# Kernel tuning notes

Measured on AMD Instinct MI355X. Metric: run time of the kernel, lower is better.

The kernel has to match this reference:

```python
import jax, jax.numpy as jnp
import numpy as np
import math

D_MODEL = 512
N_HEADS = 8
D_FF = 2048
TOP_FACTOR = 5
LN_EPS = 1e-5


def _layernorm(x, g, b):
    m = jnp.mean(x, axis=-1, keepdims=True)
    v = jnp.mean((x - m) ** 2, axis=-1, keepdims=True)
    return (x - m) / jnp.sqrt(v + LN_EPS) * g + b


def _prob_sparse_attn(q_in, k_in, v_in, wq, bq, wk, bk, wv, bv, wo, bo):
    # weights stored (in, out): y = x @ w + b  (equivalent to torch Linear)
    B, Lq, dm = q_in.shape
    Lk = k_in.shape[1]
    H, D = N_HEADS, dm // N_HEADS
    q = (q_in @ wq + bq).reshape(B, Lq, H, D).transpose(0, 2, 1, 3)  # (B,H,Lq,D)
    k = (k_in @ wk + bk).reshape(B, Lk, H, D).transpose(0, 2, 1, 3)
    v = (v_in @ wv + bv).reshape(B, Lk, H, D).transpose(0, 2, 1, 3)

    qn = q / jnp.linalg.norm(q, axis=-1, keepdims=True)
    kn = k / jnp.linalg.norm(k, axis=-1, keepdims=True)
    # full cosine-similarity matrix, reduced to a row mean (as in the original)
    scores_all = jnp.einsum('bhqd,bhkd->bhqk', qn, kn)
    mean_scores = scores_all.mean(axis=-1)  # (B,H,Lq)

    u = max(1, Lq // TOP_FACTOR)
    _, top_idx = jax.lax.top_k(mean_scores, u)  # (B,H,u)

    q_sel = jnp.take_along_axis(q, top_idx[..., None], axis=2)  # (B,H,u,D)
    scores = jnp.einsum('bhud,bhkd->bhuk', q_sel, k) / math.sqrt(D)
    attn = jax.nn.softmax(scores, axis=-1)
    ctx_sel = jnp.einsum('bhuk,bhkd->bhud', attn, v)  # (B,H,u,D)

    b_ix = jnp.arange(B)[:, None, None]
    h_ix = jnp.arange(H)[None, :, None]
    context = jnp.zeros((B, H, Lq, D), dtype=q.dtype).at[b_ix, h_ix, top_idx].set(ctx_sel)
    out = context.transpose(0, 2, 1, 3).reshape(B, Lq, dm)
    return out @ wo + bo


def _decoder_layer(x, enc_out, p):
    xn = _layernorm(x, p['ln1_g'], p['ln1_b'])
    x = x + _prob_sparse_attn(xn, xn, xn, p['sa_wq'], p['sa_bq'], p['sa_wk'], p['sa_bk'],
                              p['sa_wv'], p['sa_bv'], p['sa_wo'], p['sa_bo'])
    xn = _layernorm(x, p['ln2_g'], p['ln2_b'])
    x = x + _prob_sparse_attn(xn, enc_out, enc_out, p['ca_wq'], p['ca_bq'], p['ca_wk'], p['ca_bk'],
                              p['ca_wv'], p['ca_bv'], p['ca_wo'], p['ca_bo'])
    xn = _layernorm(x, p['ln3_g'], p['ln3_b'])
    h = jax.nn.relu(xn @ p['ff_w1'] + p['ff_b1'])
    return x + (h @ p['ff_w2'] + p['ff_b2'])


def setup_inputs() -> dict:
    key = jax.random.key(0)
    ks = iter(jax.random.split(key, 32))
    B, L = 2, 2048
    dm, dff = D_MODEL, D_FF
    s = 1.0 / math.sqrt(dm)
    inp = {
        'x': jax.random.normal(next(ks), (B, L, dm), jnp.float32),
        'enc_out': jax.random.normal(next(ks), (B, L, dm), jnp.float32),
    }
    for pre in ('sa', 'ca'):
        for nm in ('wq', 'wk', 'wv', 'wo'):
            inp[f'{pre}_{nm}'] = jax.random.normal(next(ks), (dm, dm), jnp.float32) * s
            inp[f'{pre}_{nm[1:] and "b" + nm[1:]}'] = jnp.zeros((dm,), jnp.float32)
    inp['ff_w1'] = jax.random.normal(next(ks), (dm, dff), jnp.float32) * s
    inp['ff_b1'] = jnp.zeros((dff,), jnp.float32)
    inp['ff_w2'] = jax.random.normal(next(ks), (dff, dm), jnp.float32) / math.sqrt(dff)
    inp['ff_b2'] = jnp.zeros((dm,), jnp.float32)
    for i in (1, 2, 3):
        inp[f'ln{i}_g'] = jnp.ones((dm,), jnp.float32)
        inp[f'ln{i}_b'] = jnp.zeros((dm,), jnp.float32)
    return inp


def reference(x, enc_out,
              sa_wq, sa_bq, sa_wk, sa_bk, sa_wv, sa_bv, sa_wo, sa_bo,
              ca_wq, ca_bq, ca_wk, ca_bk, ca_wv, ca_bv, ca_wo, ca_bo,
              ff_w1, ff_b1, ff_w2, ff_b2,
              ln1_g, ln1_b, ln2_g, ln2_b, ln3_g, ln3_b):
    p = dict(sa_wq=sa_wq, sa_bq=sa_bq, sa_wk=sa_wk, sa_bk=sa_bk, sa_wv=sa_wv, sa_bv=sa_bv,
             sa_wo=sa_wo, sa_bo=sa_bo, ca_wq=ca_wq, ca_bq=ca_bq, ca_wk=ca_wk, ca_bk=ca_bk,
             ca_wv=ca_wv, ca_bv=ca_bv, ca_wo=ca_wo, ca_bo=ca_bo,
             ff_w1=ff_w1, ff_b1=ff_b1, ff_w2=ff_w2, ff_b2=ff_b2,
             ln1_g=ln1_g, ln1_b=ln1_b, ln2_g=ln2_g, ln2_b=ln2_b, ln3_g=ln3_g, ln3_b=ln3_b)
    return _decoder_layer(x, enc_out, p)
```

## Files before the change

### kernel.cpp

```cpp
#include <hip/hip_runtime.h>

#define BB 2
#define LL 2048
#define DM 512
#define NH 8
#define DH 64
#define DFF 2048
#define UU 409
#define ROWS (BB*LL)
#define X_ELEMS 2097152
#define IN_TOTAL 8398336
#define NCHUNK 16

typedef unsigned short u16;
typedef __attribute__((ext_vector_type(8))) short short8;
typedef __attribute__((ext_vector_type(4))) float floatx4;

#define G_TOTAL 34700000
__device__ float g_buf[G_TOTAL];
__device__ int   g_isbf16;

#define A_XN    8398336
#define A_Q     10495488
#define A_K     12592640
#define A_V     14689792
#define A_CTX   16786944
#define A_ENC   18884096
#define A_H     20981248
#define A_MKN   23078400
#define A_MS    23079424
#define A_SEL   23112192
#define A_PARTK 23144960
#define A_LIST  23177728
#define A_PART2 23184384
#define A_WT    30426112
#define XN_H    16796672
#define XN_L    18893824
#define CTX_H   33573888
#define CTX_L   35671040
#define ENC_H   37768192
#define ENC_L   39865344
#define AH_H    41962496
#define WT_SAQKV 60852224
#define WT_SAO   62425088
#define WT_CAQ   62949376
#define WT_CAKV  63473664
#define WT_CAO   64522240
#define WT_W1    65046528
#define WT_W2    67143680

__constant__ int c_end[28] = {
    2097152, 4194304, 4456448, 4456960, 4719104, 4719616, 4981760, 4982272,
    5244416, 5244928, 5507072, 5507584, 5769728, 5770240, 6032384, 6032896,
    6295040, 6295552, 7344128, 7346176, 8394752, 8395264, 8395776, 8396288,
    8396800, 8397312, 8397824, 8398336
};

__device__ __forceinline__ float bf2f(u16 x) {
    union { unsigned int u; float f; } c; c.u = ((unsigned int)x) << 16; return c.f;
}
__device__ __forceinline__ u16 f2bf(float f) {
    union { float f; unsigned int u; } c; c.f = f;
    unsigned int u = c.u;
    return (u16)((u + 0x7FFFu + ((u >> 16) & 1u)) >> 16);
}

struct P28 { const void* p[28]; };
struct I3 { int v[3]; };
__global__ void cvt_all(P28 ps) {
    const int f = (((const u16*)ps.p[22])[0] == 0x3F80u) ? 1 : 0;
    if (blockIdx.x == 0 && threadIdx.x == 0) g_isbf16 = f;
    int stride = gridDim.x * blockDim.x;
    u16* gb16 = (u16*)g_buf;
    for (int idx = blockIdx.x * blockDim.x + threadIdx.x; idx < IN_TOTAL; idx += stride) {
        int s = 0;
        while (idx >= c_end[s]) s++;
        int start = (s == 0) ? 0 : c_end[s - 1];
        int local = idx - start;
        float v;
        if (f) v = bf2f(((const u16*)ps.p[s])[local]);
        else   v = ((const float*)ps.p[s])[local];
        g_buf[idx] = v;
        if (s == 1) {
            u16 hi = f2bf(v);
            gb16[ENC_H + local] = hi;
            gb16[ENC_L + local] = f2bf(v - bf2f(hi));
        }
    }
}

__constant__ int tj[10][6] = {
    {4194304, WT_SAQKV, 0,    512,  786432, 8},
    {4456960, WT_SAQKV, 512,  512,  786432, 8},
    {4719616, WT_SAQKV, 1024, 512,  786432, 8},
    {4982272, WT_SAO,   0,    512,  262144, 8},
    {5244928, WT_CAQ,   0,    512,  262144, 8},
    {5507584, WT_CAKV,  0,    512,  524288, 8},
    {5770240, WT_CAKV,  512,  512,  524288, 8},
    {6032896, WT_CAO,   0,    512,  262144, 8},
    {6295552, WT_W1,    0,    512, 1048576, 32},
    {7346176, WT_W2,    0,   2048, 1048576, 8},
};
__constant__ int tcum[10] = {64, 128, 192, 256, 320, 384, 448, 512, 768, 1024};
__global__ void transpose_all() {
    int bid = blockIdx.x;
    int j = 0;
    while (bid >= tcum[j]) j++;
    int t = bid - (j ? tcum[j - 1] : 0);
    int w_off = tj[j][0], wt = tj[j][1], col0 = tj[j][2];
    int K = tj[j][3], lo = tj[j][4], txn = tj[j][5];
    int Nsrc = txn * 64;
    int n0 = (t % txn) * 64, k0 = (t / txn) * 64;
    __shared__ float tb[64][65];
    int c = threadIdx.x & 63, r0 = threadIdx.x >> 6;
    const float* W = g_buf + w_off;
    u16* WTh = ((u16*)g_buf) + wt;
    for (int i = 0; i < 16; i++) {
        int r = r0 + 4 * i;
        tb[r][c] = W[(size_t)(k0 + r) * Nsrc + n0 + c];
    }
    __syncthreads();
    for (int i = 0; i < 16; i++) {
        int r = r0 + 4 * i;
        float v = tb[c][r];
        u16 hi = f2bf(v);
        size_t o = (size_t)(col0 + n0 + r) * K + k0 + c;
        WTh[o] = hi;
        WTh[lo + o] = f2bf(v - bf2f(hi));
    }
}

__global__ void lnorm_k(int x_off, int g_off, int b_off, int yh_u16, int yl_u16) {
    int row = blockIdx.x;
    int tid = threadIdx.x;
    const float* x = g_buf + x_off + (size_t)row * DM;
    float a = x[tid], c = x[tid + 256];
    float s1 = a + c, s2 = a * a + c * c;
    for (int o = 32; o > 0; o >>= 1) { s1 += __shfl_xor(s1, o); s2 += __shfl_xor(s2, o); }
    __shared__ float r1[4], r2[4];
    int wave = tid >> 6, lane = tid & 63;
    if (lane == 0) { r1[wave] = s1; r2[wave] = s2; }
    __syncthreads();
    s1 = r1[0] + r1[1] + r1[2] + r1[3];
    s2 = r2[0] + r2[1] + r2[2] + r2[3];
    float mean = s1 * (1.0f / DM);
    float var  = s2 * (1.0f / DM) - mean * mean;
    float rstd = rsqrtf(var + 1e-5f);
    const float* gg = g_buf + g_off;
    const float* bb = g_buf + b_off;
    u16* yh = ((u16*)g_buf) + yh_u16 + (size_t)row * DM;
    u16* yl = ((u16*)g_buf) + yl_u16 + (size_t)row * DM;
    float v1 = (a - mean) * rstd * gg[tid]       + bb[tid];
    float v2 = (c - mean) * rstd * gg[tid + 256] + bb[tid + 256];
    u16 h1 = f2bf(v1), h2 = f2bf(v2);
    yh[tid] = h1;       yl[tid] = f2bf(v1 - bf2f(h1));
    yh[tid + 256] = h2; yl[tid + 256] = f2bf(v2 - bf2f(h2));
}

template<int WM, bool SPLIT, bool SEC, bool RELU, bool RESID, bool FINAL, bool OUTH>
__global__ void mgemm_k(int a_u16, int wt_u16_off, I3 boffs, int resid_off,
                        int out_off, void* __restrict__ dext, int M, int N, int K) {
    constexpr int BT_M = WM * 32;
    __shared__ u16 Ash[BT_M * 40];
    __shared__ u16 Asl[SPLIT ? BT_M * 40 : 8];
    __shared__ u16 Bsh[128 * 40];
    __shared__ u16 Bsl[SPLIT ? 128 * 40 : 8];
    const u16* Ah = ((const u16*)g_buf) + a_u16;
    const u16* Al = Ah + (size_t)M * K;
    const u16* WTh = ((const u16*)g_buf) + wt_u16_off;
    const u16* WTl = WTh + (size_t)N * K;
    int isbf = FINAL ? g_isbf16 : 0;
    int tid = threadIdx.x;
    int lane = tid & 63, wid = tid >> 6;
    int wm = wid >> 1, wn = wid & 1;
    int quad = lane >> 4, l15 = lane & 15;
    int m0 = blockIdx.y * BT_M, n0 = blockIdx.x * 128;
    floatx4 acc[WM][4];
#pragma unroll
    for (int i = 0; i < WM; i++)
#pragma unroll
        for (int j = 0; j < 4; j++) acc[i][j] = (floatx4){0.f, 0.f, 0.f, 0.f};
    for (int k0 = 0; k0 < K; k0 += 32) {
#pragma unroll
        for (int i = 0; i < WM / 2; i++) {
            int idx8 = tid + 256 * i;
            int r = idx8 >> 2, c8 = (idx8 & 3) * 8;
            *(uint4*)(&Ash[r * 40 + c8]) = *(const uint4*)(Ah + (size_t)(m0 + r) * K + k0 + c8);
            if constexpr (SPLIT)
                *(uint4*)(&Asl[r * 40 + c8]) = *(const uint4*)(Al + (size_t)(m0 + r) * K + k0 + c8);
        }
#pragma unroll
        for (int i = 0; i < 2; i++) {
            int idx8 = tid + 256 * i;
            int r = idx8 >> 2, c8 = (idx8 & 3) * 8;
            *(uint4*)(&Bsh[r * 40 + c8]) = *(const uint4*)(WTh + (size_t)(n0 + r) * K + k0 + c8);
            if constexpr (SPLIT)
                *(uint4*)(&Bsl[r * 40 + c8]) = *(const uint4*)(WTl + (size_t)(n0 + r) * K + k0 + c8);
        }
        __syncthreads();
        short8 ah[WM], bh[4], al[WM], bl[4];
#pragma unroll
        for (int i = 0; i < WM; i++) {
            int ro = (wm * WM * 16 + i * 16 + l15) * 40 + quad * 8;
            ah[i] = *(const short8*)(&Ash[ro]);
            if constexpr (SPLIT) al[i] = *(const short8*)(&Asl[ro]);
        }
#pragma unroll
        for (int j = 0; j < 4; j++) {
            int ro = (wn * 64 + j * 16 + l15) * 40 + quad * 8;
            bh[j] = *(const short8*)(&Bsh[ro]);
            if constexpr (SPLIT) bl[j] = *(const short8*)(&Bsl[ro]);
        }
#pragma unroll
        for (int i = 0; i < WM; i++)
#pragma unroll
            for (int j = 0; j < 4; j++) {
                acc[i][j] = __builtin_amdgcn_mfma_f32_16x16x32_bf16(ah[i], bh[j], acc[i][j], 0, 0, 0);
                if constexpr (SPLIT) {
                    acc[i][j] = __builtin_amdgcn_mfma_f32_16x16x32_bf16(ah[i], bl[j], acc[i][j], 0, 0, 0);
                    acc[i][j] = __builtin_amdgcn_mfma_f32_16x16x32_bf16(al[i], bh[j], acc[i][j], 0, 0, 0);
                }
            }
        __syncthreads();
    }
#pragma unroll
    for (int i = 0; i < WM; i++)
#pragma unroll
        for (int j = 0; j < 4; j++)
#pragma unroll
            for (int r = 0; r < 4; r++) {
                int row = m0 + wm * WM * 16 + i * 16 + quad * 4 + r;
                int col = n0 + wn * 64 + j * 16 + l15;
                int sec = SEC ? (col >> 9) : 0;
                int ci  = SEC ? (col & 511) : col;
                float v = acc[i][j][r] + g_buf[boffs.v[sec] + ci];
                if (RELU) v = fmaxf(v, 0.f);
                if (RESID) v += g_buf[resid_off + (size_t)row * N + col];
                if (FINAL) {
                    if (isbf) ((u16*)dext)[(size_t)row * N + col] = f2bf(v);
                    else      ((float*)dext)[(size_t)row * N + col] = v;
                } else if (OUTH) {
                    ((u16*)g_buf)[out_off + (size_t)row * N + col] = f2bf(v);
                } else if (SEC) {
                    g_buf[out_off + ((size_t)sec * M + row) * 512 + ci] = v;
                } else {
                    g_buf[out_off + (size_t)row * N + col] = v;
                }
            }
}

__global__ void meankn_p1(int k_off, int part_off) {
    int bh = blockIdx.x >> 5, chunk = blockIdx.x & 31;
    int b = bh >> 3, h = bh & 7;
    int wave = threadIdx.x >> 6, lane = threadIdx.x & 63;
    const float* base = g_buf + k_off + (size_t)b * LL * DM + (size_t)h * DH + lane;
    float acc = 0.f;
    for (int t = 0; t < 16; t++) {
        int j = chunk * 64 + wave * 16 + t;
        float kv = base[(size_t)j * DM];
        float s = kv * kv;
        for (int o = 32; o > 0; o >>= 1) s += __shfl_xor(s, o);
        acc += kv / sqrtf(fmaxf(s, 1e-30f));
    }
    __shared__ float red[4][64];
    red[wave][lane] = acc;
    __syncthreads();
    if (threadIdx.x < 64)
        g_buf[part_off + (size_t)blockIdx.x * 64 + threadIdx.x] =
            red[0][threadIdx.x] + red[1][threadIdx.x] + red[2][threadIdx.x] + red[3][threadIdx.x];
}
__global__ void meankn_p2(int part_off, int mkn_off) {
    int bh = blockIdx.x; int lane = threadIdx.x;
    float s = 0.f;
    for (int c = 0; c < 32; c++) s += g_buf[part_off + (size_t)(bh * 32 + c) * 64 + lane];
    g_buf[mkn_off + bh * 64 + lane] = s * (1.0f / LL);
}

__global__ void mscore_k(int q_off, int mkn_off, int ms_off) {
    int row = blockIdx.x * 4 + (threadIdx.x >> 6);
    int lane = threadIdx.x & 63;
    int q = row & (LL - 1);
    int bh = row >> 11;
    int b = bh >> 3, h = bh & 7;
    float qv = g_buf[q_off + ((size_t)b * LL + q) * DM + h * DH + lane];
    float m = g_buf[mkn_off + bh * 64 + lane];
    float s = qv * qv, d = qv * m;
    for (int o = 32; o > 0; o >>= 1) { s += __shfl_xor(s, o); d += __shfl_xor(d, o); }
    if (lane == 0) g_buf[ms_off + row] = d / sqrtf(fmaxf(s, 1e-30f));
}

__global__ void topsel_k(int ms_off, int sel_off, int u) {
    __shared__ float s[LL];
    int bh = blockIdx.y, chunk = blockIdx.x;
    for (int i = threadIdx.x; i < LL; i += 256) s[i] = g_buf[ms_off + bh * LL + i];
    __syncthreads();
    int il = threadIdx.x >> 2;
    int i = chunk * 64 + il;
    int jq = threadIdx.x & 3;
    float si = s[i];
    int cnt = 0;
    for (int t = 0; t < 512; t++) {
        int j = jq * 512 + t;
        float sj = s[j];
        cnt += (sj > si) || (sj == si && j < i);
    }
    cnt += __shfl_xor(cnt, 1);
    cnt += __shfl_xor(cnt, 2);
    if (jq == 0) ((int*)(g_buf + sel_off))[bh * LL + i] = (cnt < u) ? 1 : 0;
}

__global__ void compact_k(int sel_off, int list_off) {
    __shared__ int cnts[256];
    __shared__ int pref[256];
    int bh = blockIdx.x, tid = threadIdx.x;
    const int* sel = (const int*)(g_buf + sel_off) + bh * LL;
    int* list = (int*)(g_buf + list_off) + bh * 416;
    int c = 0;
    for (int j = 0; j < 8; j++) c += sel[tid * 8 + j];
    cnts[tid] = c;
    __syncthreads();
    if (tid == 0) { int run = 0; for (int i = 0; i < 256; i++) { pref[i] = run; run += cnts[i]; } }
    __syncthreads();
    int base = pref[tid];
    for (int j = 0; j < 8; j++) {
        int i = tid * 8 + j;
        if (sel[i]) list[base++] = i;
    }
}

__global__ void zero_k(int off, int n) {
    int i = blockIdx.x * blockDim.x + threadIdx.x;
    int st = gridDim.x * blockDim.x;
    for (; i < n; i += st) g_buf[off + i] = 0.f;
}

__global__ void attn_flash(int q_off, int k_off, int v_off, int list_off, int part_off, int u) {
    int bh = blockIdx.y, b = bh >> 3, h = bh & 7;
    int chunk = blockIdx.z;
    int tid = threadIdx.x, lane = tid & 63, w = tid >> 6;
    int quad = lane >> 4, l15 = lane & 15;
    const int* list = (const int*)(g_buf + list_off);

    int slot_q = blockIdx.x * 64 + w * 16 + l15;
    int qidx = list[bh * 416 + (slot_q < u ? slot_q : u - 1)];
    const float* qp = g_buf + q_off + ((size_t)b * LL + qidx) * DM + h * DH;
    short8 qh[2], ql[2];
#pragma unroll
    for (int d2 = 0; d2 < 2; d2++) {
        float v[8] __attribute__((aligned(16)));
        *(float4*)(v)     = *(const float4*)(qp + d2 * 32 + quad * 8);
        *(float4*)(v + 4) = *(const float4*)(qp + d2 * 32 + quad * 8 + 4);
        u16 hh[8] __attribute__((aligned(16)));
        u16 lo[8] __attribute__((aligned(16)));
#pragma unroll
        for (int j = 0; j < 8; j++) {
            float s = v[j] * 0.125f;
            u16 hi = f2bf(s); hh[j] = hi; lo[j] = f2bf(s - bf2f(hi));
        }
        qh[d2] = *(const short8*)hh; ql[d2] = *(const short8*)lo;
    }

    __shared__ u16 Ksh[64 * 72], Ksl[64 * 72];
    __shared__ u16 Vth[64 * 72], Vtl[64 * 72];
    __shared__ float Ps[4][16 * 68];

    float m_run[4] = {-3.0e38f, -3.0e38f, -3.0e38f, -3.0e38f};
    float l_run[4] = {0.f, 0.f, 0.f, 0.f};
    floatx4 acc_o[4];
#pragma unroll
    for (int j = 0; j < 4; j++) acc_o[j] = (floatx4){0.f, 0.f, 0.f, 0.f};

    for (int kt = 0; kt < 2; kt++) {
        int row0 = chunk * 128 + kt * 64;
        {
            int r = tid >> 2, c = (tid & 3) * 16;
            const float* kp = g_buf + k_off + ((size_t)b * LL + row0 + r) * DM + h * DH + c;
            float v[16] __attribute__((aligned(16)));
            *(float4*)(v)      = *(const float4*)(kp);
            *(float4*)(v + 4)  = *(const float4*)(kp + 4);
            *(float4*)(v + 8)  = *(const float4*)(kp + 8);
            *(float4*)(v + 12) = *(const float4*)(kp + 12);
            u16 hh[16] __attribute__((aligned(16)));
            u16 lo[16] __attribute__((aligned(16)));
#pragma unroll
            for (int j = 0; j < 16; j++) { u16 hi = f2bf(v[j]); hh[j] = hi; lo[j] = f2bf(v[j] - bf2f(hi)); }
            *(uint4*)(&Ksh[r * 72 + c])     = ((const uint4*)hh)[0];
            *(uint4*)(&Ksh[r * 72 + c + 8]) = ((const uint4*)hh)[1];
            *(uint4*)(&Ksl[r * 72 + c])     = ((const uint4*)lo)[0];
            *(uint4*)(&Ksl[r * 72 + c + 8]) = ((const uint4*)lo)[1];
        }
#pragma unroll
        for (int it = 0; it < 2; it++) {
            int sl = it * 256 + tid;
            int d = sl & 63, oct = sl >> 6;
            const float* vp = g_buf + v_off + ((size_t)b * LL + row0 + oct * 8) * DM + h * DH + d;
            u16 hh[8] __attribute__((aligned(16)));
            u16 lo[8] __attribute__((aligned(16)));
#pragma unroll
            for (int i = 0; i < 8; i++) {
                float x = vp[(size_t)i * DM];
                u16 hi = f2bf(x); hh[i] = hi; lo[i] = f2bf(x - bf2f(hi));
            }
            *(uint4*)(&Vth[d * 72 + oct * 8]) = *(const uint4*)hh;
            *(uint4*)(&Vtl[d * 72 + oct * 8]) = *(const uint4*)lo;
        }
        __syncthreads();
        floatx4 sacc[4];
#pragma unroll
        for (int t = 0; t < 4; t++) {
            sacc[t] = (floatx4){0.f, 0.f, 0.f, 0.f};
#pragma unroll
            for (int d2 = 0; d2 < 2; d2++) {
                int ro = (t * 16 + l15) * 72 + d2 * 32 + quad * 8;
                short8 kh = *(const short8*)(&Ksh[ro]);
                short8 kl = *(const short8*)(&Ksl[ro]);
                sacc[t] = __builtin_amdgcn_mfma_f32_16x16x32_bf16(qh[d2], kh, sacc[t], 0, 0, 0);
                sacc[t] = __builtin_amdgcn_mfma_f32_16x16x32_bf16(qh[d2], kl, sacc[t], 0, 0, 0);
                sacc[t] = __builtin_amdgcn_mfma_f32_16x16x32_bf16(ql[d2], kh, sacc[t], 0, 0, 0);
            }
        }
        float alpha[4];
#pragma unroll
        for (int r = 0; r < 4; r++) {
            float mx = fmaxf(fmaxf(sacc[0][r], sacc[1][r]), fmaxf(sacc[2][r], sacc[3][r]));
            for (int o = 1; o < 16; o <<= 1) mx = fmaxf(mx, __shfl_xor(mx, o));
            float mn = fmaxf(m_run[r], mx);
            alpha[r] = __expf(m_run[r] - mn);
            m_run[r] = mn;
            float ls = 0.f;
#pragma unroll
            for (int t = 0; t < 4; t++) {
                float p = __expf(sacc[t][r] - mn);
                sacc[t][r] = p;
                ls += p;
            }
            for (int o = 1; o < 16; o <<= 1) ls += __shfl_xor(ls, o);
            l_run[r] = l_run[r] * alpha[r] + ls;
        }
#pragma unroll
        for (int t = 0; t < 4; t++)
#pragma unroll
            for (int r = 0; r < 4; r++)
                Ps[w][(quad * 4 + r) * 68 + t * 16 + l15] = sacc[t][r];
#pragma unroll
        for (int j = 0; j < 4; j++)
#pragma unroll
            for (int r = 0; r < 4; r++) acc_o[j][r] *= alpha[r];
#pragma unroll
        for (int s2 = 0; s2 < 2; s2++) {
            float pv[8] __attribute__((aligned(16)));
            *(float4*)(pv)     = *(const float4*)(&Ps[w][l15 * 68 + s2 * 32 + quad * 8]);
            *(float4*)(pv + 4) = *(const float4*)(&Ps[w][l15 * 68 + s2 * 32 + quad * 8 + 4]);
            u16 ph[8] __attribute__((aligned(16)));
            u16 pl[8] __attribute__((aligned(16)));
#pragma unroll
            for (int j = 0; j < 8; j++) { u16 hi = f2bf(pv[j]); ph[j] = hi; pl[j] = f2bf(pv[j] - bf2f(hi)); }
            short8 phv = *(const short8*)ph, plv = *(const short8*)pl;
#pragma unroll
            for (int j = 0; j < 4; j++) {
                int ro = (j * 16 + l15) * 72 + s2 * 32 + quad * 8;
                short8 vh = *(const short8*)(&Vth[ro]);
                short8 vl = *(const short8*)(&Vtl[ro]);
                acc_o[j] = __builtin_amdgcn_mfma_f32_16x16x32_bf16(phv, vh, acc_o[j], 0, 0, 0);
                acc_o[j] = __builtin_amdgcn_mfma_f32_16x16x32_bf16(phv, vl, acc_o[j], 0, 0, 0);
                acc_o[j] = __builtin_amdgcn_mfma_f32_16x16x32_bf16(plv, vh, acc_o[j], 0, 0, 0);
            }
        }
        __syncthreads();
    }
#pragma unroll
    for (int r = 0; r < 4; r++) {
        int slot = blockIdx.x * 64 + w * 16 + quad * 4 + r;
        if (slot >= u) continue;
        float* pp = g_buf + part_off + (((size_t)bh * 416 + slot) * NCHUNK + chunk) * 68;
#pragma unroll
        for (int j = 0; j < 4; j++) pp[j * 16 + l15] = acc_o[j][r];
        if (l15 == 0) { pp[64] = m_run[r]; pp[65] = l_run[r]; }
    }
}

__global__ void attn_combine(int part_off, int list_off, int u) {
    int bh = blockIdx.y;
    int b = bh >> 3, h = bh & 7;
    int tid = threadIdx.x;
    int qi = tid >> 4;
    int kb = tid & 15;
    int ds = kb * 4;
    int slot = blockIdx.x * 16 + qi;
    if (slot >= u) return;
    int qidx = ((const int*)(g_buf + list_off))[bh * 416 + slot];
    const float* pp = g_buf + part_off + ((size_t)bh * 416 + slot) * NCHUNK * 68;
    float m = -3.0e38f;
#pragma unroll
    for (int c = 0; c < NCHUNK; c++) m = fmaxf(m, pp[c * 68 + 64]);
    float l = 0.f, O0 = 0.f, O1 = 0.f, O2 = 0.f, O3 = 0.f;
#pragma unroll
    for (int c = 0; c < NCHUNK; c++) {
        float a = __expf(pp[c * 68 + 64] - m);
        l += a * pp[c * 68 + 65];
        float4 o = *(const float4*)(pp + c * 68 + ds);
        O0 += a * o.x; O1 += a * o.y; O2 += a * o.z; O3 += a * o.w;
    }
    float inv = 1.0f / l;
    float o0 = O0 * inv, o1 = O1 * inv, o2 = O2 * inv, o3 = O3 * inv;
    size_t idx = ((size_t)b * LL + qidx) * DM + h * DH + ds;
    ushort4 hv, lv;
    hv.x = f2bf(o0); lv.x = f2bf(o0 - bf2f(hv.x));
    hv.y = f2bf(o1); lv.y = f2bf(o1 - bf2f(hv.y));
    hv.z = f2bf(o2); lv.z = f2bf(o2 - bf2f(hv.z));
    hv.w = f2bf(o3); lv.w = f2bf(o3 - bf2f(hv.w));
    *(ushort4*)(((u16*)g_buf) + CTX_H + idx) = hv;
    *(ushort4*)(((u16*)g_buf) + CTX_L + idx) = lv;
}

extern "C" void kernel_launch(void* const* d_in, const int* in_sizes, int n_in,
                              void* d_out, int out_size, void* d_ws, size_t ws_size,
                              hipStream_t stream) {
    static const int SZ[28] = {
        2097152, 2097152,
        262144, 512, 262144, 512, 262144, 512, 262144, 512,
        262144, 512, 262144, 512, 262144, 512, 262144, 512,
        1048576, 2048, 1048576, 512,
        512, 512, 512, 512, 512, 512
    };
    int OFF[28];
    int cur = 0;
    for (int i = 0; i < 28; i++) { OFF[i] = cur; cur += SZ[i]; }
    const int X = X_ELEMS;

    P28 ps;
    for (int i = 0; i < 28; i++) ps.p[i] = d_in[i];
    cvt_all<<<4096, 256, 0, stream>>>(ps);
    transpose_all<<<1024, 256, 0, stream>>>();

    auto select_attend = [&](void) {
        meankn_p1<<<16 * 32, 256, 0, stream>>>(A_K, A_PARTK);
        meankn_p2<<<16, 64, 0, stream>>>(A_PARTK, A_MKN);
        mscore_k<<<(BB * NH * LL) / 4, 256, 0, stream>>>(A_Q, A_MKN, A_MS);
        topsel_k<<<dim3(32, 16), 256, 0, stream>>>(A_MS, A_SEL, UU);
        compact_k<<<BB * NH, 256, 0, stream>>>(A_SEL, A_LIST);
        zero_k<<<1024, 256, 0, stream>>>(A_CTX, X);
        attn_flash<<<dim3(7, 16, NCHUNK), 256, 0, stream>>>(A_Q, A_K, A_V, A_LIST, A_PART2, UU);
        attn_combine<<<dim3(26, 16), 256, 0, stream>>>(A_PART2, A_LIST, UU);
    };

    lnorm_k<<<ROWS, 256, 0, stream>>>(OFF[0], OFF[22], OFF[23], XN_H, XN_L);
    mgemm_k<2, true, true, false, false, false, false><<<dim3(12, 64), 256, 0, stream>>>(
        XN_H, WT_SAQKV, I3{{OFF[3], OFF[5], OFF[7]}}, 0, A_Q, nullptr, ROWS, 1536, 512);
    select_attend();
    mgemm_k<2, true, false, false, true, false, false><<<dim3(4, 64), 256, 0, stream>>>(
        CTX_H, WT_SAO, I3{{OFF[9], 0, 0}}, OFF[0], OFF[0], nullptr, ROWS, 512, 512);

    lnorm_k<<<ROWS, 256, 0, stream>>>(OFF[0], OFF[24], OFF[25], XN_H, XN_L);
    mgemm_k<2, true, false, false, false, false, false><<<dim3(4, 64), 256, 0, stream>>>(
        XN_H, WT_CAQ, I3{{OFF[11], 0, 0}}, 0, A_Q, nullptr, ROWS, 512, 512);
    mgemm_k<2, true, true, false, false, false, false><<<dim3(8, 64), 256, 0, stream>>>(
        ENC_H, WT_CAKV, I3{{OFF[13], OFF[15], 0}}, 0, A_K, nullptr, ROWS, 1024, 512);
    select_attend();
    mgemm_k<2, false, false, false, true, false, false><<<dim3(4, 64), 256, 0, stream>>>(
        CTX_H, WT_CAO, I3{{OFF[17], 0, 0}}, OFF[0], OFF[0], nullptr, ROWS, 512, 512);

    lnorm_k<<<ROWS, 256, 0, stream>>>(OFF[0], OFF[26], OFF[27], XN_H, XN_L);
    mgemm_k<4, false, false, true, false, false, true><<<dim3(16, 32), 256, 0, stream>>>(
        XN_H, WT_W1, I3{{OFF[19], 0, 0}}, 0, AH_H, nullptr, ROWS, 2048, 512);
    mgemm_k<2, false, false, false, true, true, false><<<dim3(4, 64), 256, 0, stream>>>(
        AH_H, WT_W2, I3{{OFF[21], 0, 0}}, OFF[0], 0, d_out, ROWS, 512, 2048);
}
```

Measured before the change: 591.4 us.

## Precompute split-bf16 K and transposed V once; widen attention blocks; shrink GEMM M-tiles

Adds a prep kernel that converts K into hi/lo bf16 pairs and V into transposed hi/lo bf16 once per head. Before this, each attention chunk block repeated that conversion and did strided V loads for every query group. The flash kernel now handles two 16-query groups per wave (128 queries per block), so each K/V tile staged in shared memory is reused across twice as many queries, and it loads the precomputed tiles with vector copies. The N=512 GEMMs switch to 32-row tiles to get more blocks onto the device. The cost is extra global buffers, one more launch per attention, higher register pressure in the flash kernel, and fewer attention blocks.

```diff
diff --git a/kernel.cpp b/kernel.cpp
--- a/kernel.cpp
+++ b/kernel.cpp
@@ -16,7 +16,7 @@
 typedef __attribute__((ext_vector_type(8))) short short8;
 typedef __attribute__((ext_vector_type(4))) float floatx4;
 
-#define G_TOTAL 34700000
+#define G_TOTAL 38900000
 __device__ float g_buf[G_TOTAL];
 __device__ int   g_isbf16;
 
@@ -48,6 +48,10 @@
 #define WT_CAO   64522240
 #define WT_W1    65046528
 #define WT_W2    67143680
+#define KH_U    69240832
+#define KL_U    71337984
+#define VTH_U   73435136
+#define VTL_U   75532288
 
 __constant__ int c_end[28] = {
     2097152, 4194304, 4456448, 4456960, 4719104, 4719616, 4981760, 4982272,
@@ -161,6 +165,7 @@
 __global__ void mgemm_k(int a_u16, int wt_u16_off, I3 boffs, int resid_off,
                         int out_off, void* __restrict__ dext, int M, int N, int K) {
     constexpr int BT_M = WM * 32;
+    constexpr int A4 = BT_M * 4;
     __shared__ u16 Ash[BT_M * 40];
     __shared__ u16 Asl[SPLIT ? BT_M * 40 : 8];
     __shared__ u16 Bsh[128 * 40];
@@ -182,12 +187,14 @@
         for (int j = 0; j < 4; j++) acc[i][j] = (floatx4){0.f, 0.f, 0.f, 0.f};
     for (int k0 = 0; k0 < K; k0 += 32) {
 #pragma unroll
-        for (int i = 0; i < WM / 2; i++) {
+        for (int i = 0; i < (A4 + 255) / 256; i++) {
             int idx8 = tid + 256 * i;
-            int r = idx8 >> 2, c8 = (idx8 & 3) * 8;
-            *(uint4*)(&Ash[r * 40 + c8]) = *(const uint4*)(Ah + (size_t)(m0 + r) * K + k0 + c8);
-            if constexpr (SPLIT)
-                *(uint4*)(&Asl[r * 40 + c8]) = *(const uint4*)(Al + (size_t)(m0 + r) * K + k0 + c8);
+            if (A4 % 256 == 0 || idx8 < A4) {
+                int r = idx8 >> 2, c8 = (idx8 & 3) * 8;
+                *(uint4*)(&Ash[r * 40 + c8]) = *(const uint4*)(Ah + (size_t)(m0 + r) * K + k0 + c8);
+                if constexpr (SPLIT)
+                    *(uint4*)(&Asl[r * 40 + c8]) = *(const uint4*)(Al + (size_t)(m0 + r) * K + k0 + c8);
+            }
         }
 #pragma unroll
         for (int i = 0; i < 2; i++) {
@@ -249,6 +256,50 @@
             }
 }
 
+__global__ void prep_attn(int k_off, int v_off) {
+    int kb = blockIdx.x, bh = blockIdx.y;
+    int b = bh >> 3, h = bh & 7;
+    int tid = threadIdx.x;
+    int tok = tid >> 2, c = (tid & 3) * 16;
+    u16* KH = (u16*)g_buf + KH_U + (size_t)bh * LL * 64;
+    u16* KL = (u16*)g_buf + KL_U + (size_t)bh * LL * 64;
+    u16* VTH = (u16*)g_buf + VTH_U + (size_t)bh * 64 * LL;
+    u16* VTL = (u16*)g_buf + VTL_U + (size_t)bh * 64 * LL;
+    {
+        const float* kp = g_buf + k_off + ((size_t)(b * LL + kb * 64 + tok)) * DM + h * DH + c;
+        float v[16] __attribute__((aligned(16)));
+#pragma unroll
+        for (int i = 0; i < 4; i++) *(float4*)(v + 4 * i) = *(const float4*)(kp + 4 * i);
+        u16 hh[16] __attribute__((aligned(16)));
+        u16 lo[16] __attribute__((aligned(16)));
+#pragma unroll
+        for (int i = 0; i < 16; i++) { u16 hi = f2bf(v[i]); hh[i] = hi; lo[i] = f2bf(v[i] - bf2f(hi)); }
+        size_t o = (size_t)(kb * 64 + tok) * 64 + c;
+        *(uint4*)(&KH[o]) = ((const uint4*)hh)[0]; *(uint4*)(&KH[o + 8]) = ((const uint4*)hh)[1];
+        *(uint4*)(&KL[o]) = ((const uint4*)lo)[0]; *(uint4*)(&KL[o + 8]) = ((const uint4*)lo)[1];
+    }
+    __shared__ float vt[64][65];
+    {
+        const float* vp = g_buf + v_off + ((size_t)(b * LL + kb * 64 + tok)) * DM + h * DH + c;
+#pragma unroll
+        for (int i = 0; i < 16; i++) vt[tok][c + i] = vp[i];
+    }
+    __syncthreads();
+    {
+        int d = tid >> 2, ck = (tid & 3) * 16;
+        u16 hh[16] __attribute__((aligned(16)));
+        u16 lo[16] __attribute__((aligned(16)));
+#pragma unroll
+        for (int i = 0; i < 16; i++) {
+            float x = vt[ck + i][d];
+            u16 hi = f2bf(x); hh[i] = hi; lo[i] = f2bf(x - bf2f(hi));
+        }
+        size_t o = (size_t)d * LL + kb * 64 + ck;
+        *(uint4*)(&VTH[o]) = ((const uint4*)hh)[0]; *(uint4*)(&VTH[o + 8]) = ((const uint4*)hh)[1];
+        *(uint4*)(&VTL[o]) = ((const uint4*)lo)[0]; *(uint4*)(&VTL[o + 8]) = ((const uint4*)lo)[1];
+    }
+}
+
 __global__ void meankn_p1(int k_off, int part_off) {
     int bh = blockIdx.x >> 5, chunk = blockIdx.x & 31;
     int b = bh >> 3, h = bh & 7;
@@ -334,149 +385,150 @@
     for (; i < n; i += st) g_buf[off + i] = 0.f;
 }
 
-__global__ void attn_flash(int q_off, int k_off, int v_off, int list_off, int part_off, int u) {
+__global__ void attn_flash(int q_off, int list_off, int part_off, int u) {
     int bh = blockIdx.y, b = bh >> 3, h = bh & 7;
     int chunk = blockIdx.z;
     int tid = threadIdx.x, lane = tid & 63, w = tid >> 6;
     int quad = lane >> 4, l15 = lane & 15;
     const int* list = (const int*)(g_buf + list_off);
 
-    int slot_q = blockIdx.x * 64 + w * 16 + l15;
-    int qidx = list[bh * 416 + (slot_q < u ? slot_q : u - 1)];
-    const float* qp = g_buf + q_off + ((size_t)b * LL + qidx) * DM + h * DH;
-    short8 qh[2], ql[2];
-#pragma unroll
-    for (int d2 = 0; d2 < 2; d2++) {
-        float v[8] __attribute__((aligned(16)));
-        *(float4*)(v)     = *(const float4*)(qp + d2 * 32 + quad * 8);
-        *(float4*)(v + 4) = *(const float4*)(qp + d2 * 32 + quad * 8 + 4);
-        u16 hh[8] __attribute__((aligned(16)));
-        u16 lo[8] __attribute__((aligned(16)));
-#pragma unroll
-        for (int j = 0; j < 8; j++) {
-            float s = v[j] * 0.125f;
-            u16 hi = f2bf(s); hh[j] = hi; lo[j] = f2bf(s - bf2f(hi));
-        }
-        qh[d2] = *(const short8*)hh; ql[d2] = *(const short8*)lo;
-    }
-
-    __shared__ u16 Ksh[64 * 72], Ksl[64 * 72];
-    __shared__ u16 Vth[64 * 72], Vtl[64 * 72];
+    short8 qh[2][2], ql[2][2];
+#pragma unroll
+    for (int g = 0; g < 2; g++) {
+        int slot_q = blockIdx.x * 128 + w * 32 + g * 16 + l15;
+        int qidx = list[bh * 416 + (slot_q < u ? slot_q : u - 1)];
+        const float* qp = g_buf + q_off + ((size_t)b * LL + qidx) * DM + h * DH;
+#pragma unroll
+        for (int d2 = 0; d2 < 2; d2++) {
+            float v[8] __attribute__((aligned(16)));
+            *(float4*)(v)     = *(const float4*)(qp + d2 * 32 + quad * 8);
+            *(float4*)(v + 4) = *(const float4*)(qp + d2 * 32 + quad * 8 + 4);
+            u16 hh[8] __attribute__((aligned(16)));
+            u16 lo[8] __attribute__((aligned(16)));
+#pragma unroll
+            for (int j = 0; j < 8; j++) {
+                float s = v[j] * 0.125f;
+                u16 hi = f2bf(s); hh[j] = hi; lo[j] = f2bf(s - bf2f(hi));
+            }
+            qh[g][d2] = *(const short8*)hh; ql[g][d2] = *(const short8*)lo;
+        }
+    }
+
+    __shared__ u16 Ksh[64 * 68], Ksl[64 * 68];
+    __shared__ u16 Vth[64 * 68], Vtl[64 * 68];
     __shared__ float Ps[4][16 * 68];
 
-    float m_run[4] = {-3.0e38f, -3.0e38f, -3.0e38f, -3.0e38f};
-    float l_run[4] = {0.f, 0.f, 0.f, 0.f};
-    floatx4 acc_o[4];
-#pragma unroll
-    for (int j = 0; j < 4; j++) acc_o[j] = (floatx4){0.f, 0.f, 0.f, 0.f};
+    float m_run[2][4], l_run[2][4];
+    floatx4 acc_o[2][4];
+#pragma unroll
+    for (int g = 0; g < 2; g++)
+#pragma unroll
+        for (int r = 0; r < 4; r++) { m_run[g][r] = -3.0e38f; l_run[g][r] = 0.f; }
+#pragma unroll
+    for (int g = 0; g < 2; g++)
+#pragma unroll
+        for (int j = 0; j < 4; j++) acc_o[g][j] = (floatx4){0.f, 0.f, 0.f, 0.f};
+
+    const u16* KHp = (const u16*)g_buf + KH_U + (size_t)bh * LL * 64;
+    const u16* KLp = (const u16*)g_buf + KL_U + (size_t)bh * LL * 64;
+    const u16* VTHp = (const u16*)g_buf + VTH_U + (size_t)bh * 64 * LL;
+    const u16* VTLp = (const u16*)g_buf + VTL_U + (size_t)bh * 64 * LL;
 
     for (int kt = 0; kt < 2; kt++) {
         int row0 = chunk * 128 + kt * 64;
         {
             int r = tid >> 2, c = (tid & 3) * 16;
-            const float* kp = g_buf + k_off + ((size_t)b * LL + row0 + r) * DM + h * DH + c;
-            float v[16] __attribute__((aligned(16)));
-            *(float4*)(v)      = *(const float4*)(kp);
-            *(float4*)(v + 4)  = *(const float4*)(kp + 4);
-            *(float4*)(v + 8)  = *(const float4*)(kp + 8);
-            *(float4*)(v + 12) = *(const float4*)(kp + 12);
-            u16 hh[16] __attribute__((aligned(16)));
-            u16 lo[16] __attribute__((aligned(16)));
-#pragma unroll
-            for (int j = 0; j < 16; j++) { u16 hi = f2bf(v[j]); hh[j] = hi; lo[j] = f2bf(v[j] - bf2f(hi)); }
-            *(uint4*)(&Ksh[r * 72 + c])     = ((const uint4*)hh)[0];
-            *(uint4*)(&Ksh[r * 72 + c + 8]) = ((const uint4*)hh)[1];
-            *(uint4*)(&Ksl[r * 72 + c])     = ((const uint4*)lo)[0];
-            *(uint4*)(&Ksl[r * 72 + c + 8]) = ((const uint4*)lo)[1];
-        }
-#pragma unroll
-        for (int it = 0; it < 2; it++) {
-            int sl = it * 256 + tid;
-            int d = sl & 63, oct = sl >> 6;
-            const float* vp = g_buf + v_off + ((size_t)b * LL + row0 + oct * 8) * DM + h * DH + d;
-            u16 hh[8] __attribute__((aligned(16)));
-            u16 lo[8] __attribute__((aligned(16)));
-#pragma unroll
-            for (int i = 0; i < 8; i++) {
-                float x = vp[(size_t)i * DM];
-                u16 hi = f2bf(x); hh[i] = hi; lo[i] = f2bf(x - bf2f(hi));
+            const u16* s1 = KHp + (size_t)(row0 + r) * 64 + c;
+            const u16* s2 = KLp + (size_t)(row0 + r) * 64 + c;
+            *(uint4*)(&Ksh[r * 68 + c])     = *(const uint4*)(s1);
+            *(uint4*)(&Ksh[r * 68 + c + 8]) = *(const uint4*)(s1 + 8);
+            *(uint4*)(&Ksl[r * 68 + c])     = *(const uint4*)(s2);
+            *(uint4*)(&Ksl[r * 68 + c + 8]) = *(const uint4*)(s2 + 8);
+            const u16* s3 = VTHp + (size_t)r * LL + row0 + c;
+            const u16* s4 = VTLp + (size_t)r * LL + row0 + c;
+            *(uint4*)(&Vth[r * 68 + c])     = *(const uint4*)(s3);
+            *(uint4*)(&Vth[r * 68 + c + 8]) = *(const uint4*)(s3 + 8);
+            *(uint4*)(&Vtl[r * 68 + c])     = *(const uint4*)(s4);
+            *(uint4*)(&Vtl[r * 68 + c + 8]) = *(const uint4*)(s4 + 8);
+        }
+        __syncthreads();
+#pragma unroll
+        for (int g = 0; g < 2; g++) {
+            floatx4 sacc[4];
+#pragma unroll
+            for (int t = 0; t < 4; t++) {
+                sacc[t] = (floatx4){0.f, 0.f, 0.f, 0.f};
+#pragma unroll
+                for (int d2 = 0; d2 < 2; d2++) {
+                    int ro = (t * 16 + l15) * 68 + d2 * 32 + quad * 8;
+                    short8 kh = *(const short8*)(&Ksh[ro]);
+                    short8 kl = *(const short8*)(&Ksl[ro]);
+                    sacc[t] = __builtin_amdgcn_mfma_f32_16x16x32_bf16(qh[g][d2], kh, sacc[t], 0, 0, 0);
+                    sacc[t] = __builtin_amdgcn_mfma_f32_16x16x32_bf16(qh[g][d2], kl, sacc[t], 0, 0, 0);
+                    sacc[t] = __builtin_amdgcn_mfma_f32_16x16x32_bf16(ql[g][d2], kh, sacc[t], 0, 0, 0);
+                }
             }
-            *(uint4*)(&Vth[d * 72 + oct * 8]) = *(const uint4*)hh;
-            *(uint4*)(&Vtl[d * 72 + oct * 8]) = *(const uint4*)lo;
+            float alpha[4];
+#pragma unroll
+            for (int r = 0; r < 4; r++) {
+                float mx = fmaxf(fmaxf(sacc[0][r], sacc[1][r]), fmaxf(sacc[2][r], sacc[3][r]));
+                for (int o = 1; o < 16; o <<= 1) mx = fmaxf(mx, __shfl_xor(mx, o));
+                float mn = fmaxf(m_run[g][r], mx);
+                alpha[r] = __expf(m_run[g][r] - mn);
+                m_run[g][r] = mn;
+                float ls = 0.f;
+#pragma unroll
+                for (int t = 0; t < 4; t++) {
+                    float p = __expf(sacc[t][r] - mn);
+                    sacc[t][r] = p;
+                    ls += p;
+                }
+                for (int o = 1; o < 16; o <<= 1) ls += __shfl_xor(ls, o);
+                l_run[g][r] = l_run[g][r] * alpha[r] + ls;
+            }
+#pragma unroll
+            for (int t = 0; t < 4; t++)
+#pragma unroll
+                for (int r = 0; r < 4; r++)
+                    Ps[w][(quad * 4 + r) * 68 + t * 16 + l15] = sacc[t][r];
+#pragma unroll
+            for (int j = 0; j < 4; j++)
+#pragma unroll
+                for (int r = 0; r < 4; r++) acc_o[g][j][r] *= alpha[r];
+#pragma unroll
+            for (int s2 = 0; s2 < 2; s2++) {
+                float pv[8] __attribute__((aligned(16)));
+                *(float4*)(pv)     = *(const float4*)(&Ps[w][l15 * 68 + s2 * 32 + quad * 8]);
+                *(float4*)(pv + 4) = *(const float4*)(&Ps[w][l15 * 68 + s2 * 32 + quad * 8 + 4]);
+                u16 ph[8] __attribute__((aligned(16)));
+                u16 pl[8] __attribute__((aligned(16)));
+#pragma unroll
+                for (int j = 0; j < 8; j++) { u16 hi = f2bf(pv[j]); ph[j] = hi; pl[j] = f2bf(pv[j] - bf2f(hi)); }
+                short8 phv = *(const short8*)ph, plv = *(const short8*)pl;
+#pragma unroll
+                for (int j = 0; j < 4; j++) {
+                    int ro = (j * 16 + l15) * 68 + s2 * 32 + quad * 8;
+                    short8 vh = *(const short8*)(&Vth[ro]);
+                    short8 vl = *(const short8*)(&Vtl[ro]);
+                    acc_o[g][j] = __builtin_amdgcn_mfma_f32_16x16x32_bf16(phv, vh, acc_o[g][j], 0, 0, 0);
+                    acc_o[g][j] = __builtin_amdgcn_mfma_f32_16x16x32_bf16(phv, vl, acc_o[g][j], 0, 0, 0);
+                    acc_o[g][j] = __builtin_amdgcn_mfma_f32_16x16x32_bf16(plv, vh, acc_o[g][j], 0, 0, 0);
+                }
+            }
         }
         __syncthreads();
-        floatx4 sacc[4];
-#pragma unroll
-        for (int t = 0; t < 4; t++) {
-            sacc[t] = (floatx4){0.f, 0.f, 0.f, 0.f};
-#pragma unroll
-            for (int d2 = 0; d2 < 2; d2++) {
-                int ro = (t * 16 + l15) * 72 + d2 * 32 + quad * 8;
-                short8 kh = *(const short8*)(&Ksh[ro]);
-                short8 kl = *(const short8*)(&Ksl[ro]);
-                sacc[t] = __builtin_amdgcn_mfma_f32_16x16x32_bf16(qh[d2], kh, sacc[t], 0, 0, 0);
-                sacc[t] = __builtin_amdgcn_mfma_f32_16x16x32_bf16(qh[d2], kl, sacc[t], 0, 0, 0);
-                sacc[t] = __builtin_amdgcn_mfma_f32_16x16x32_bf16(ql[d2], kh, sacc[t], 0, 0, 0);
-            }
-        }
-        float alpha[4];
+    }
+#pragma unroll
+    for (int g = 0; g < 2; g++)
 #pragma unroll
         for (int r = 0; r < 4; r++) {
-            float mx = fmaxf(fmaxf(sacc[0][r], sacc[1][r]), fmaxf(sacc[2][r], sacc[3][r]));
-            for (int o = 1; o < 16; o <<= 1) mx = fmaxf(mx, __shfl_xor(mx, o));
-            float mn = fmaxf(m_run[r], mx);
-            alpha[r] = __expf(m_run[r] - mn);
-            m_run[r] = mn;
-            float ls = 0.f;
-#pragma unroll
-            for (int t = 0; t < 4; t++) {
-                float p = __expf(sacc[t][r] - mn);
-                sacc[t][r] = p;
-                ls += p;
-            }
-            for (int o = 1; o < 16; o <<= 1) ls += __shfl_xor(ls, o);
-            l_run[r] = l_run[r] * alpha[r] + ls;
-        }
-#pragma unroll
-        for (int t = 0; t < 4; t++)
-#pragma unroll
-            for (int r = 0; r < 4; r++)
-                Ps[w][(quad * 4 + r) * 68 + t * 16 + l15] = sacc[t][r];
-#pragma unroll
-        for (int j = 0; j < 4; j++)
-#pragma unroll
-            for (int r = 0; r < 4; r++) acc_o[j][r] *= alpha[r];
-#pragma unroll
-        for (int s2 = 0; s2 < 2; s2++) {
-            float pv[8] __attribute__((aligned(16)));
-            *(float4*)(pv)     = *(const float4*)(&Ps[w][l15 * 68 + s2 * 32 + quad * 8]);
-            *(float4*)(pv + 4) = *(const float4*)(&Ps[w][l15 * 68 + s2 * 32 + quad * 8 + 4]);
-            u16 ph[8] __attribute__((aligned(16)));
-            u16 pl[8] __attribute__((aligned(16)));
-#pragma unroll
-            for (int j = 0; j < 8; j++) { u16 hi = f2bf(pv[j]); ph[j] = hi; pl[j] = f2bf(pv[j] - bf2f(hi)); }
-            short8 phv = *(const short8*)ph, plv = *(const short8*)pl;
-#pragma unroll
-            for (int j = 0; j < 4; j++) {
-                int ro = (j * 16 + l15) * 72 + s2 * 32 + quad * 8;
-                short8 vh = *(const short8*)(&Vth[ro]);
-                short8 vl = *(const short8*)(&Vtl[ro]);
-                acc_o[j] = __builtin_amdgcn_mfma_f32_16x16x32_bf16(phv, vh, acc_o[j], 0, 0, 0);
-                acc_o[j] = __builtin_amdgcn_mfma_f32_16x16x32_bf16(phv, vl, acc_o[j], 0, 0, 0);
-                acc_o[j] = __builtin_amdgcn_mfma_f32_16x16x32_bf16(plv, vh, acc_o[j], 0, 0, 0);
-            }
-        }
-        __syncthreads();
-    }
-#pragma unroll
-    for (int r = 0; r < 4; r++) {
-        int slot = blockIdx.x * 64 + w * 16 + quad * 4 + r;
-        if (slot >= u) continue;
-        float* pp = g_buf + part_off + (((size_t)bh * 416 + slot) * NCHUNK + chunk) * 68;
-#pragma unroll
-        for (int j = 0; j < 4; j++) pp[j * 16 + l15] = acc_o[j][r];
-        if (l15 == 0) { pp[64] = m_run[r]; pp[65] = l_run[r]; }
-    }
+            int slot = blockIdx.x * 128 + w * 32 + g * 16 + quad * 4 + r;
+            if (slot >= u) continue;
+            float* pp = g_buf + part_off + (((size_t)bh * 416 + slot) * NCHUNK + chunk) * 68;
+#pragma unroll
+            for (int j = 0; j < 4; j++) pp[j * 16 + l15] = acc_o[g][j][r];
+            if (l15 == 0) { pp[64] = m_run[g][r]; pp[65] = l_run[g][r]; }
+        }
 }
 
 __global__ void attn_combine(int part_off, int list_off, int u) {
@@ -534,13 +586,14 @@
     transpose_all<<<1024, 256, 0, stream>>>();
 
     auto select_attend = [&](void) {
+        prep_attn<<<dim3(32, 16), 256, 0, stream>>>(A_K, A_V);
         meankn_p1<<<16 * 32, 256, 0, stream>>>(A_K, A_PARTK);
         meankn_p2<<<16, 64, 0, stream>>>(A_PARTK, A_MKN);
         mscore_k<<<(BB * NH * LL) / 4, 256, 0, stream>>>(A_Q, A_MKN, A_MS);
         topsel_k<<<dim3(32, 16), 256, 0, stream>>>(A_MS, A_SEL, UU);
         compact_k<<<BB * NH, 256, 0, stream>>>(A_SEL, A_LIST);
         zero_k<<<1024, 256, 0, stream>>>(A_CTX, X);
-        attn_flash<<<dim3(7, 16, NCHUNK), 256, 0, stream>>>(A_Q, A_K, A_V, A_LIST, A_PART2, UU);
+        attn_flash<<<dim3(4, 16, NCHUNK), 256, 0, stream>>>(A_Q, A_LIST, A_PART2, UU);
         attn_combine<<<dim3(26, 16), 256, 0, stream>>>(A_PART2, A_LIST, UU);
     };
 
@@ -548,21 +601,21 @@
     mgemm_k<2, true, true, false, false, false, false><<<dim3(12, 64), 256, 0, stream>>>(
         XN_H, WT_SAQKV, I3{{OFF[3], OFF[5], OFF[7]}}, 0, A_Q, nullptr, ROWS, 1536, 512);
     select_attend();
-    mgemm_k<2, true, false, false, true, false, false><<<dim3(4, 64), 256, 0, stream>>>(
+    mgemm_k<1, true, false, false, true, false, false><<<dim3(4, 128), 256, 0, stream>>>(
         CTX_H, WT_SAO, I3{{OFF[9], 0, 0}}, OFF[0], OFF[0], nullptr, ROWS, 512, 512);
 
     lnorm_k<<<ROWS, 256, 0, stream>>>(OFF[0], OFF[24], OFF[25], XN_H, XN_L);
-    mgemm_k<2, true, false, false, false, false, false><<<dim3(4, 64), 256, 0, stream>>>(
+    mgemm_k<1, true, false, false, false, false, false><<<dim3(4, 128), 256, 0, stream>>>(
         XN_H, WT_CAQ, I3{{OFF[11], 0, 0}}, 0, A_Q, nullptr, ROWS, 512, 512);
     mgemm_k<2, true, true, false, false, false, false><<<dim3(8, 64), 256, 0, stream>>>(
         ENC_H, WT_CAKV, I3{{OFF[13], OFF[15], 0}}, 0, A_K, nullptr, ROWS, 1024, 512);
     select_attend();
-    mgemm_k<2, false, false, false, true, false, false><<<dim3(4, 64), 256, 0, stream>>>(
+    mgemm_k<1, false, false, false, true, false, false><<<dim3(4, 128), 256, 0, stream>>>(
         CTX_H, WT_CAO, I3{{OFF[17], 0, 0}}, OFF[0], OFF[0], nullptr, ROWS, 512, 512);
 
     lnorm_k<<<ROWS, 256, 0, stream>>>(OFF[0], OFF[26], OFF[27], XN_H, XN_L);
     mgemm_k<4, false, false, true, false, false, true><<<dim3(16, 32), 256, 0, stream>>>(
         XN_H, WT_W1, I3{{OFF[19], 0, 0}}, 0, AH_H, nullptr, ROWS, 2048, 512);
-    mgemm_k<2, false, false, false, true, true, false><<<dim3(4, 64), 256, 0, stream>>>(
+    mgemm_k<1, false, false, false, true, true, false><<<dim3(4, 128), 256, 0, stream>>>(
         AH_H, WT_W2, I3{{OFF[21], 0, 0}}, OFF[0], 0, d_out, ROWS, 512, 2048);
 }
```

Result: slower. 652.4 us (+10.3%).
